# Performance work log

Measured on AMD Instinct MI355X. Metric: run time of the kernel, lower is better.

Reference implementation:

```python
import jax, jax.numpy as jnp
import numpy as np

EPS = 1e-12  # torch F.normalize default eps

def l2norm(h):
    # torch.nn.functional.normalize(h, dim=1): x / max(||x||_2, eps)
    n = jnp.sqrt(jnp.sum(h * h, axis=1, keepdims=True))
    return h / jnp.maximum(n, EPS)

def setup_inputs() -> dict:
    key = jax.random.key(0)
    k1, k2, k3, k4, k5 = jax.random.split(key, 5)
    N, D, E, HOPS = 50000, 128, 600000, 3
    x = jax.random.normal(k1, (N, D), dtype=jnp.float32)
    edge_index = jax.random.randint(k2, (2, E), 0, N, dtype=jnp.int64)
    attn_w = jax.random.normal(k3, (HOPS, 2 * D), dtype=jnp.float32) * 0.05
    attn_b = jax.random.normal(k4, (HOPS,), dtype=jnp.float32) * 0.05
    noise = jax.random.normal(k5, (HOPS, N, D), dtype=jnp.float32)
    return {"x": x, "edge_index": edge_index, "attn_w": attn_w,
            "attn_b": attn_b, "noise": noise}

def reference(x, edge_index, attn_w, attn_b, noise):
    N = x.shape[0]
    sigma = 0.1
    src = edge_index[0]  # A[src, dst] = alpha; after transpose, aggr[dst] += alpha * h[src]
    dst = edge_index[1]
    outs = [l2norm(x)]
    num_hops = attn_w.shape[0]
    for k in range(num_hops):
        h = outs[-1]
        hs = h[src]                          # [E, D]
        hd = h[dst]                          # [E, D]
        # edge MLP: Linear(2D,1) + SELU, then sigmoid
        e = hs @ attn_w[k, : h.shape[1]] + hd @ attn_w[k, h.shape[1]:] + attn_b[k]  # [E]
        alpha = jax.nn.sigmoid(jax.nn.selu(e))  # [E]
        msg = alpha[:, None] * hs               # [E, D]
        aggr = jax.ops.segment_sum(msg, dst, num_segments=N)  # [N, D]
        noised = aggr + sigma * noise[k]
        outs.append(l2norm(noised))
    return jnp.stack(outs)  # [num_hops+1, N, D]
```

## Files before the change

### kernel.cpp

```cpp
#include <hip/hip_runtime.h>
#include <hip/hip_fp16.h>
#include <math.h>

#define EPSN 1e-12f
#define CAP 64

__device__ __forceinline__ float wave_sum(float v) {
#pragma unroll
  for (int o = 32; o >= 1; o >>= 1) v += __shfl_xor(v, o);
  return v;
}

__device__ __forceinline__ float edge_alpha(float e) {
  const float SC = 1.0507009873554805f;
  const float AL = 1.6732632423543772f;
  float se = e > 0.f ? SC * e : SC * AL * (__expf(e) - 1.f);
  return 1.f / (1.f + __expf(-se));
}

__global__ __launch_bounds__(256) void prep_kernel(const int* __restrict__ ei,
                                                   const float* __restrict__ x,
                                                   const float* __restrict__ attn_w,
                                                   int* __restrict__ cursor,
                                                   int* __restrict__ slots,
                                                   float* __restrict__ out0,
                                                   __half2* __restrict__ hb0,
                                                   float* __restrict__ p1, float* __restrict__ p2,
                                                   int N, int E) {
  int tid = blockIdx.x * 256 + threadIdx.x;
  int T = gridDim.x * 256;
  for (int e = tid; e < E; e += T) {
    int d = ei[E + e];
    int pos = atomicAdd(&cursor[d], 1);
    if (pos < CAP) slots[(size_t)d * CAP + pos] = ei[e];
  }
  int lane = threadIdx.x & 63;
  int gw = tid >> 6;
  int TW = T >> 6;
  const float2* x2 = (const float2*)x;
  for (int wid = gw; wid < N; wid += TW) {
    float2 v = x2[(size_t)wid * 64 + lane];
    float ss = wave_sum(v.x * v.x + v.y * v.y);
    float inv = 1.f / fmaxf(sqrtf(ss), EPSN);
    v.x *= inv; v.y *= inv;
    float* op = out0 + (size_t)wid * 128 + lane * 2;
    __builtin_nontemporal_store(v.x, op);
    __builtin_nontemporal_store(v.y, op + 1);
    hb0[(size_t)wid * 64 + lane] = __floats2half2_rn(v.x, v.y);
    float d1 = wave_sum(v.x * attn_w[2 * lane] + v.y * attn_w[2 * lane + 1]);
    float d2 = wave_sum(v.x * attn_w[128 + 2 * lane] + v.y * attn_w[128 + 2 * lane + 1]);
    if (lane == 0) { p1[wid] = d1; p2[wid] = d2; }
  }
}

__global__ __launch_bounds__(256) void hop_kernel(const __half2* __restrict__ hb,
                                                  const float* __restrict__ p1,
                                                  const float* __restrict__ p2,
                                                  const int* __restrict__ counts,
                                                  const int* __restrict__ slots,
                                                  const float* __restrict__ noise_k,
                                                  const float* __restrict__ attn_b, int k,
                                                  float* __restrict__ out_next,
                                                  __half2* __restrict__ hb_next,
                                                  float* __restrict__ np1, float* __restrict__ np2,
                                                  const float* __restrict__ wnext,
                                                  int N, int last) {
  int wid = (int)((blockIdx.x * blockDim.x + threadIdx.x) >> 6);
  int lane = threadIdx.x & 63;
  if (wid >= N) return;
  int cnt = counts[wid]; if (cnt > CAP) cnt = CAP;
  float p2d = p2[wid] + attn_b[k];
  float a0 = 0.f, a1 = 0.f;

  int s_l = 0; float al_l = 0.f;
  if (lane < cnt) {
    s_l = slots[(size_t)wid * CAP + lane];
    al_l = edge_alpha(p1[s_l] + p2d);
  }
  int j = 0;
  for (; j + 4 <= cnt; j += 4) {
    int s0 = __shfl(s_l, j), s1 = __shfl(s_l, j + 1);
    int s2 = __shfl(s_l, j + 2), s3 = __shfl(s_l, j + 3);
    float A0 = __shfl(al_l, j), A1 = __shfl(al_l, j + 1);
    float A2 = __shfl(al_l, j + 2), A3 = __shfl(al_l, j + 3);
    float2 v0 = __half22float2(hb[(size_t)s0 * 64 + lane]);
    float2 v1 = __half22float2(hb[(size_t)s1 * 64 + lane]);
    float2 v2 = __half22float2(hb[(size_t)s2 * 64 + lane]);
    float2 v3 = __half22float2(hb[(size_t)s3 * 64 + lane]);
    a0 += A0 * v0.x; a1 += A0 * v0.y;
    a0 += A1 * v1.x; a1 += A1 * v1.y;
    a0 += A2 * v2.x; a1 += A2 * v2.y;
    a0 += A3 * v3.x; a1 += A3 * v3.y;
  }
  for (; j < cnt; ++j) {
    int s = __shfl(s_l, j);
    float A = __shfl(al_l, j);
    float2 v = __half22float2(hb[(size_t)s * 64 + lane]);
    a0 += A * v.x; a1 += A * v.y;
  }

  const float* nr = noise_k + (size_t)wid * 128 + lane * 2;
  a0 += 0.1f * __builtin_nontemporal_load(nr);
  a1 += 0.1f * __builtin_nontemporal_load(nr + 1);
  float ss = wave_sum(a0 * a0 + a1 * a1);
  float inv = 1.f / fmaxf(sqrtf(ss), EPSN);
  a0 *= inv; a1 *= inv;
  float* op = out_next + (size_t)wid * 128 + lane * 2;
  __builtin_nontemporal_store(a0, op);
  __builtin_nontemporal_store(a1, op + 1);
  if (!last) {
    hb_next[(size_t)wid * 64 + lane] = __floats2half2_rn(a0, a1);
    float d1 = wave_sum(a0 * wnext[2 * lane] + a1 * wnext[2 * lane + 1]);
    float d2 = wave_sum(a0 * wnext[128 + 2 * lane] + a1 * wnext[128 + 2 * lane + 1]);
    if (lane == 0) { np1[wid] = d1; np2[wid] = d2; }
  }
}

extern "C" void kernel_launch(void* const* d_in, const int* in_sizes, int n_in,
                              void* d_out, int out_size, void* d_ws, size_t ws_size,
                              hipStream_t stream) {
  const float* x      = (const float*)d_in[0];
  const int*   ei     = (const int*)d_in[1];
  const float* attn_w = (const float*)d_in[2];
  const float* attn_b = (const float*)d_in[3];
  const float* noise  = (const float*)d_in[4];
  float* out = (float*)d_out;

  const int N = in_sizes[0] / 128;
  const int E = in_sizes[1] / 2;
  const int HOPS = in_sizes[3];

  auto align = [](size_t v) { return (v + 255) & ~size_t(255); };
  char* w = (char*)d_ws;
  int* cursor   = (int*)w; w += align((size_t)N * 4);
  int* slots    = (int*)w; w += align((size_t)N * CAP * 4);
  float* pA1 = (float*)w; w += align((size_t)N * 4);
  float* pA2 = (float*)w; w += align((size_t)N * 4);
  float* pB1 = (float*)w; w += align((size_t)N * 4);
  float* pB2 = (float*)w; w += align((size_t)N * 4);
  __half2* hbA = (__half2*)w; w += align((size_t)N * 64 * 4);
  __half2* hbB = (__half2*)w; w += align((size_t)N * 64 * 4);

  hipMemsetAsync(cursor, 0, (size_t)N * 4, stream);

  prep_kernel<<<2048, 256, 0, stream>>>(ei, x, attn_w, cursor, slots,
                                        out, hbA, pA1, pA2, N, E);

  int wbl = (N + 3) / 4;
  float* p1b[2] = {pA1, pB1};
  float* p2b[2] = {pA2, pB2};
  __half2* hbb[2] = {hbA, hbB};
  for (int k = 0; k < HOPS; ++k) {
    int cur = k & 1, nxt = cur ^ 1;
    int last = (k == HOPS - 1) ? 1 : 0;
    const float* wnext = last ? attn_w : (attn_w + (size_t)(k + 1) * 256);
    hop_kernel<<<wbl, 256, 0, stream>>>(hbb[cur],
                                        p1b[cur], p2b[cur],
                                        cursor, slots,
                                        noise + (size_t)k * N * 128, attn_b, k,
                                        out + (size_t)(k + 1) * N * 128,
                                        hbb[nxt],
                                        p1b[nxt], p2b[nxt], wnext,
                                        N, last);
  }
}
```

Measured before the change: 329.0 us.

## Split wave into four 16-lane groups gathering neighbor rows with 16-byte loads

The hop kernel now splits each 64-lane wave into four 16-lane groups, each handling a different neighbor edge and loading a full 256-byte fp16 row as int4 per lane. Partial sums are combined across groups with cross-lane shuffles, then one group does the noise add, normalization, output stores and next-hop projections using 8 values per lane. The aim is fewer, wider gather load instructions and more independent edges in flight per wave. In exchange it adds a cross-group shuffle reduction and leaves three quarters of the wave idle during the epilogue.

Result: no change. 325.8 us (-1.0%).

```diff
diff --git a/kernel.cpp b/kernel.cpp
--- a/kernel.cpp
+++ b/kernel.cpp
@@ -68,51 +68,91 @@
   int wid = (int)((blockIdx.x * blockDim.x + threadIdx.x) >> 6);
   int lane = threadIdx.x & 63;
   if (wid >= N) return;
+  int g = lane >> 4;
+  int l = lane & 15;
   int cnt = counts[wid]; if (cnt > CAP) cnt = CAP;
   float p2d = p2[wid] + attn_b[k];
-  float a0 = 0.f, a1 = 0.f;
 
   int s_l = 0; float al_l = 0.f;
   if (lane < cnt) {
     s_l = slots[(size_t)wid * CAP + lane];
     al_l = edge_alpha(p1[s_l] + p2d);
   }
-  int j = 0;
-  for (; j + 4 <= cnt; j += 4) {
-    int s0 = __shfl(s_l, j), s1 = __shfl(s_l, j + 1);
-    int s2 = __shfl(s_l, j + 2), s3 = __shfl(s_l, j + 3);
-    float A0 = __shfl(al_l, j), A1 = __shfl(al_l, j + 1);
-    float A2 = __shfl(al_l, j + 2), A3 = __shfl(al_l, j + 3);
-    float2 v0 = __half22float2(hb[(size_t)s0 * 64 + lane]);
-    float2 v1 = __half22float2(hb[(size_t)s1 * 64 + lane]);
-    float2 v2 = __half22float2(hb[(size_t)s2 * 64 + lane]);
-    float2 v3 = __half22float2(hb[(size_t)s3 * 64 + lane]);
-    a0 += A0 * v0.x; a1 += A0 * v0.y;
-    a0 += A1 * v1.x; a1 += A1 * v1.y;
-    a0 += A2 * v2.x; a1 += A2 * v2.y;
-    a0 += A3 * v3.x; a1 += A3 * v3.y;
-  }
-  for (; j < cnt; ++j) {
-    int s = __shfl(s_l, j);
-    float A = __shfl(al_l, j);
-    float2 v = __half22float2(hb[(size_t)s * 64 + lane]);
-    a0 += A * v.x; a1 += A * v.y;
-  }
-
-  const float* nr = noise_k + (size_t)wid * 128 + lane * 2;
-  a0 += 0.1f * __builtin_nontemporal_load(nr);
-  a1 += 0.1f * __builtin_nontemporal_load(nr + 1);
-  float ss = wave_sum(a0 * a0 + a1 * a1);
-  float inv = 1.f / fmaxf(sqrtf(ss), EPSN);
-  a0 *= inv; a1 *= inv;
-  float* op = out_next + (size_t)wid * 128 + lane * 2;
-  __builtin_nontemporal_store(a0, op);
-  __builtin_nontemporal_store(a1, op + 1);
-  if (!last) {
-    hb_next[(size_t)wid * 64 + lane] = __floats2half2_rn(a0, a1);
-    float d1 = wave_sum(a0 * wnext[2 * lane] + a1 * wnext[2 * lane + 1]);
-    float d2 = wave_sum(a0 * wnext[128 + 2 * lane] + a1 * wnext[128 + 2 * lane + 1]);
-    if (lane == 0) { np1[wid] = d1; np2[wid] = d2; }
+
+  const int4* hb4 = (const int4*)hb;
+  float a0 = 0.f, a1 = 0.f, a2 = 0.f, a3 = 0.f, a4 = 0.f, a5 = 0.f, a6 = 0.f, a7 = 0.f;
+  int jfull = cnt & ~3;
+  for (int j = 0; j < jfull; j += 4) {
+    int jj = j + g;
+    int s = __shfl(s_l, jj);
+    float A = __shfl(al_l, jj);
+    int4 r = hb4[(size_t)s * 16 + l];
+    float2 f0 = __half22float2(*(__half2*)&r.x);
+    float2 f1 = __half22float2(*(__half2*)&r.y);
+    float2 f2 = __half22float2(*(__half2*)&r.z);
+    float2 f3 = __half22float2(*(__half2*)&r.w);
+    a0 += A * f0.x; a1 += A * f0.y; a2 += A * f1.x; a3 += A * f1.y;
+    a4 += A * f2.x; a5 += A * f2.y; a6 += A * f3.x; a7 += A * f3.y;
+  }
+  int rem = cnt - jfull;
+  if (rem) {
+    int jj = jfull + (g < rem ? g : rem - 1);
+    int s = __shfl(s_l, jj);
+    float A = __shfl(al_l, jj);
+    if (g >= rem) A = 0.f;
+    int4 r = hb4[(size_t)s * 16 + l];
+    float2 f0 = __half22float2(*(__half2*)&r.x);
+    float2 f1 = __half22float2(*(__half2*)&r.y);
+    float2 f2 = __half22float2(*(__half2*)&r.z);
+    float2 f3 = __half22float2(*(__half2*)&r.w);
+    a0 += A * f0.x; a1 += A * f0.y; a2 += A * f1.x; a3 += A * f1.y;
+    a4 += A * f2.x; a5 += A * f2.y; a6 += A * f3.x; a7 += A * f3.y;
+  }
+#pragma unroll
+  for (int off = 16; off <= 32; off <<= 1) {
+    a0 += __shfl_xor(a0, off); a1 += __shfl_xor(a1, off);
+    a2 += __shfl_xor(a2, off); a3 += __shfl_xor(a3, off);
+    a4 += __shfl_xor(a4, off); a5 += __shfl_xor(a5, off);
+    a6 += __shfl_xor(a6, off); a7 += __shfl_xor(a7, off);
+  }
+
+  if (g == 0) {
+    const float* nr = noise_k + (size_t)wid * 128 + l * 8;
+    float4 n0, n1;
+    n0.x = __builtin_nontemporal_load(nr);     n0.y = __builtin_nontemporal_load(nr + 1);
+    n0.z = __builtin_nontemporal_load(nr + 2); n0.w = __builtin_nontemporal_load(nr + 3);
+    n1.x = __builtin_nontemporal_load(nr + 4); n1.y = __builtin_nontemporal_load(nr + 5);
+    n1.z = __builtin_nontemporal_load(nr + 6); n1.w = __builtin_nontemporal_load(nr + 7);
+    a0 += 0.1f * n0.x; a1 += 0.1f * n0.y; a2 += 0.1f * n0.z; a3 += 0.1f * n0.w;
+    a4 += 0.1f * n1.x; a5 += 0.1f * n1.y; a6 += 0.1f * n1.z; a7 += 0.1f * n1.w;
+    float part = a0*a0 + a1*a1 + a2*a2 + a3*a3 + a4*a4 + a5*a5 + a6*a6 + a7*a7;
+#pragma unroll
+    for (int o = 8; o >= 1; o >>= 1) part += __shfl_xor(part, o);
+    float inv = 1.f / fmaxf(sqrtf(part), EPSN);
+    a0 *= inv; a1 *= inv; a2 *= inv; a3 *= inv;
+    a4 *= inv; a5 *= inv; a6 *= inv; a7 *= inv;
+    float* op = out_next + (size_t)wid * 128 + l * 8;
+    __builtin_nontemporal_store(a0, op);     __builtin_nontemporal_store(a1, op + 1);
+    __builtin_nontemporal_store(a2, op + 2); __builtin_nontemporal_store(a3, op + 3);
+    __builtin_nontemporal_store(a4, op + 4); __builtin_nontemporal_store(a5, op + 5);
+    __builtin_nontemporal_store(a6, op + 6); __builtin_nontemporal_store(a7, op + 7);
+    if (!last) {
+      __half2 m0 = __floats2half2_rn(a0, a1), m1 = __floats2half2_rn(a2, a3);
+      __half2 m2 = __floats2half2_rn(a4, a5), m3 = __floats2half2_rn(a6, a7);
+      int4 mv;
+      mv.x = *(int*)&m0; mv.y = *(int*)&m1; mv.z = *(int*)&m2; mv.w = *(int*)&m3;
+      ((int4*)hb_next)[(size_t)wid * 16 + l] = mv;
+      const float* w1 = wnext + l * 8;
+      const float* w2 = wnext + 128 + l * 8;
+      float d1 = a0*w1[0] + a1*w1[1] + a2*w1[2] + a3*w1[3] + a4*w1[4] + a5*w1[5] + a6*w1[6] + a7*w1[7];
+      float d2 = a0*w2[0] + a1*w2[1] + a2*w2[2] + a3*w2[3] + a4*w2[4] + a5*w2[5] + a6*w2[6] + a7*w2[7];
+#pragma unroll
+      for (int o = 8; o >= 1; o >>= 1) {
+        d1 += __shfl_xor(d1, o);
+        d2 += __shfl_xor(d2, o);
+      }
+      if (l == 0) { np1[wid] = d1; np2[wid] = d2; }
+    }
   }
 }
 
```
